# Optimization experiments

Measured on AMD Instinct MI355X. Metric: run time of the kernel, lower is better.

The kernel has to match this reference:

```python
import jax, jax.numpy as jnp
import numpy as np

EPS = 1e-10
W_SILOG, W_L2, W_BINS = 1.0, 1.0, 1.0  # w_masked=1.0 -> invalid branch skipped


def setup_inputs() -> dict:
    key = jax.random.key(0)
    k1, k2, k3, k4 = jax.random.split(key, 4)
    B, H, W = 8, 240, 320
    NB = 256  # n_bins
    prediction = jax.random.uniform(k1, (B, 1, H, W), dtype=jnp.float32)
    target = jax.random.uniform(k2, (B, 1, H, W), dtype=jnp.float32)
    bin_edges = jax.random.uniform(k3, (B, NB + 1), dtype=jnp.float32)
    mask = jax.random.randint(k4, (B, 1, H, W), 0, 2).astype(jnp.bool_)
    return {"prediction": prediction, "target": target, "bin_edges": bin_edges, "mask": mask}


def _onedirectional_dist(a, b):
    # a: [B, Na], b: [B, Nb] -> sum over Na of min_j (a_i - b_j)^2, shape [B]
    d2 = (a[:, :, None] - b[:, None, :]) ** 2  # [B, Na, Nb]
    return jnp.min(d2, axis=2).sum(axis=1)


def reference(prediction, target, bin_edges, mask):
    # Chamfer distance between bin centers and target depth values
    bin_centers = 0.5 * (bin_edges[:, :-1] + bin_edges[:, 1:])  # [B, NB]
    target_depths = target.reshape(target.shape[0], -1)         # [B, H*W]
    chamfer = (_onedirectional_dist(bin_centers, target_depths)
               + _onedirectional_dist(target_depths, bin_centers)).mean()

    # Masked reductions (equivalent to boolean-indexed means, jit-friendly)
    p = prediction.reshape(-1)
    t = target.reshape(-1)
    fm = mask.reshape(-1).astype(p.dtype)
    cnt = fm.sum()

    # L2: sqrt(MSE over masked elements)
    l2 = jnp.sqrt(jnp.sum((p - t) ** 2 * fm) / cnt)

    # SILog
    d = jnp.log(p + EPS) - jnp.log(t + EPS)
    d_mean = jnp.sum(d * fm) / cnt
    d2_mean = jnp.sum(d * d * fm) / cnt
    silog = 10.0 * jnp.sqrt(d2_mean - 0.85 * d_mean ** 2)

    return W_L2 * l2 + W_SILOG * silog + W_BINS * chamfer
```

## Files before the change

### kernel.cpp

```cpp
#include <hip/hip_runtime.h>
#include <math.h>

#define HW     76800
#define NBATCH 8
#define NB     256
#define NEDGE  257
#define ELEMS  12
#define XBLKS  25
#define MAIN_BLOCKS (XBLKS * NBATCH)
#define FINF 3.402823466e+38f


__device__ __forceinline__ double wsum64(double v) {
#pragma unroll
  for (int o = 32; o > 0; o >>= 1) v += __shfl_down(v, o, 64);
  return v;
}

__device__ __forceinline__ unsigned int nzb(unsigned int w) {
  return ((w & 0xFFu) != 0u) + (((w >> 8) & 0xFFu) != 0u) +
         (((w >> 16) & 0xFFu) != 0u) + ((w >> 24) != 0u);
}

__global__ void __launch_bounds__(256) k_prep(
    const float* __restrict__ edges, const unsigned char* __restrict__ mask,
    double* __restrict__ sums, unsigned int* __restrict__ ticket,
    unsigned int* __restrict__ flag, unsigned int* __restrict__ gD,
    float* __restrict__ cs) {
  const int tid = threadIdx.x, b = blockIdx.x;
  if (b < NBATCH) {
    __shared__ float s[NB];
    float v = 0.5f * (edges[b * NEDGE + tid] + edges[b * NEDGE + tid + 1]);
    for (int k = 2; k <= NB; k <<= 1) {
      for (int j = k >> 1; j > 0; j >>= 1) {
        float partner;
        if (j < 64) {
          partner = __shfl_xor(v, j, 64);
        } else {
          __syncthreads();
          s[tid] = v;
          __syncthreads();
          partner = s[tid ^ j];
        }
        const bool up = ((tid & k) == 0);
        const bool low = ((tid & j) == 0);
        v = (low == up) ? fminf(v, partner) : fmaxf(v, partner);
      }
    }
    cs[b * NB + tid] = v;
    gD[b * NB + tid] = 0u;
  } else {
    uint4 raw = ((const uint4*)mask)[tid];
    unsigned int c = nzb(raw.x) + nzb(raw.y) + nzb(raw.z) + nzb(raw.w);
#pragma unroll
    for (int o = 32; o > 0; o >>= 1) c += __shfl_down(c, o, 64);
    __shared__ unsigned int sh[4];
    if ((tid & 63) == 0) sh[tid >> 6] = c;
    __syncthreads();
    if (tid == 0) *flag = ((sh[0] + sh[1] + sh[2] + sh[3]) > 1024u) ? 1u : 0u;
    if (tid < 40) sums[tid] = 0.0;
    if (tid == 40) *ticket = 0u;
  }
}

__global__ void __launch_bounds__(256) k_main(
    const float* __restrict__ p, const float* __restrict__ t,
    const void* __restrict__ mask, const unsigned int* __restrict__ flag,
    const float* __restrict__ cs, double* __restrict__ sums,
    unsigned int* __restrict__ gD, unsigned int* __restrict__ ticket,
    float* __restrict__ out) {
  __shared__ float c_lds[NB];
  __shared__ unsigned int d_lds[NB];
  __shared__ double shred[4][5];
  __shared__ double fin[40];
  __shared__ unsigned int last_flag;

  const int tid = threadIdx.x, lane = tid & 63, wid = tid >> 6;
  const int b = blockIdx.y;
  const int ebase = b * HW + blockIdx.x * (NB * ELEMS) + tid * ELEMS;

  c_lds[tid] = cs[b * NB + tid];
  d_lds[tid] = 0u;
  __syncthreads();
  const float c255 = c_lds[255], c127 = c_lds[127], c63 = c_lds[63],
              c191 = c_lds[191], c31 = c_lds[31], c95 = c_lds[95],
              c159 = c_lds[159], c223 = c_lds[223];

  float pe[ELEMS], te[ELEMS];
  int me[ELEMS];
  {
    const float4* pp = (const float4*)(p + ebase);
    const float4* tt = (const float4*)(t + ebase);
#pragma unroll
    for (int q = 0; q < 3; ++q) {
      float4 a = pp[q], c = tt[q];
      pe[q * 4 + 0] = a.x; pe[q * 4 + 1] = a.y; pe[q * 4 + 2] = a.z; pe[q * 4 + 3] = a.w;
      te[q * 4 + 0] = c.x; te[q * 4 + 1] = c.y; te[q * 4 + 2] = c.z; te[q * 4 + 3] = c.w;
    }
  }
  if (*flag) {
    const unsigned int* mp = (const unsigned int*)((const unsigned char*)mask + ebase);
    unsigned int w[3] = {mp[0], mp[1], mp[2]};
#pragma unroll
    for (int e = 0; e < ELEMS; ++e) me[e] = (w[e >> 2] >> ((e & 3) * 8)) & 0xFFu;
  } else {
    const int4* mp = (const int4*)((const int*)mask + ebase);
#pragma unroll
    for (int q = 0; q < 3; ++q) {
      int4 m4 = mp[q];
      me[q * 4 + 0] = m4.x; me[q * 4 + 1] = m4.y; me[q * 4 + 2] = m4.z; me[q * 4 + 3] = m4.w;
    }
  }

  double cnt = 0, ssq = 0, sd = 0, sd2 = 0, dir2 = 0;
#pragma unroll
  for (int e = 0; e < ELEMS; ++e) {
    const float pi = pe[e], ti = te[e];
    if (me[e]) {
      float diff = pi - ti;
      float d = logf(pi + 1e-10f) - logf(ti + 1e-10f);
      cnt += 1.0;
      ssq += (double)diff * (double)diff;
      sd  += (double)d;
      sd2 += (double)d * (double)d;
    }
    int k = -1;
    if (c127 <= ti) k = 127;
    { float pr = (k == 127) ? c191 : c63; if (pr <= ti) k += 64; }
    { int idx = (k + 32) >> 6;
      float pr = (idx >= 2) ? ((idx == 3) ? c223 : c159)
                            : ((idx == 1) ? c95 : c31);
      if (pr <= ti) k += 32; }
    if (c255 <= ti) k = 255;
#pragma unroll
    for (int s = 16; s > 0; s >>= 1) {
      int nk = k + s;
      if (nk < NB && c_lds[nk] <= ti) k = nk;
    }
    float dl = (k >= 0)     ? ti - c_lds[k]     : FINF;
    float dr = (k + 1 < NB) ? c_lds[k + 1] - ti : FINF;
    if (k >= 0)     atomicMax(&d_lds[k],     ~__float_as_uint(dl));
    if (k + 1 < NB) atomicMax(&d_lds[k + 1], ~__float_as_uint(dr));
    float dmin = fminf(dl, dr);
    dir2 += (double)dmin * (double)dmin;
  }

  __syncthreads();
  {
    unsigned int dv = d_lds[tid];
    if (dv) atomicMax(&gD[b * NB + tid], dv);
  }

  double acc[5] = {cnt, ssq, sd, sd2, dir2};
#pragma unroll
  for (int i = 0; i < 5; ++i) {
    double r = wsum64(acc[i]);
    if (lane == 0) shred[wid][i] = r;
  }
  __syncthreads();
  if (tid < 5) {
    atomicAdd(&sums[b * 5 + tid],
              shred[0][tid] + shred[1][tid] + shred[2][tid] + shred[3][tid]);
  }

  asm volatile("s_waitcnt vmcnt(0) lgkmcnt(0)" ::: "memory");
  __syncthreads();
  if (tid == 0)
    last_flag = (atomicAdd(ticket, 1u) == (unsigned)(MAIN_BLOCKS - 1)) ? 1u : 0u;
  __syncthreads();
  if (last_flag == 0u) return;

  if (tid < 40) fin[tid] = atomicAdd(&sums[tid], 0.0);

  double dir1 = 0.0;
#pragma unroll
  for (int r = 0; r < 2; ++r) {
    const int bb = wid + r * 4;
    float c[4], D[4];
#pragma unroll
    for (int i = 0; i < 4; ++i) {
      const int idx = bb * NB + lane * 4 + i;
      c[i] = cs[idx];
      unsigned int s = atomicOr(&gD[idx], 0u);
      D[i] = s ? __uint_as_float(~s) : FINF;
    }

    float pa[4];
    pa[0] = D[0] - c[0];
    pa[1] = fminf(pa[0], D[1] - c[1]);
    pa[2] = fminf(pa[1], D[2] - c[2]);
    pa[3] = fminf(pa[2], D[3] - c[3]);
    float s1 = pa[3];
#pragma unroll
    for (int off = 1; off < 64; off <<= 1) {
      float u = __shfl_up(s1, off, 64);
      if (lane >= off) s1 = fminf(s1, u);
    }
    float exL = __shfl_up(s1, 1, 64);
    if (lane == 0) exL = FINF;

    float sb[4];
    sb[3] = D[3] + c[3];
    sb[2] = fminf(sb[3], D[2] + c[2]);
    sb[1] = fminf(sb[2], D[1] + c[1]);
    sb[0] = fminf(sb[1], D[0] + c[0]);
    float s2 = sb[0];
#pragma unroll
    for (int off = 1; off < 64; off <<= 1) {
      float u = __shfl_down(s2, off, 64);
      if (lane + off < 64) s2 = fminf(s2, u);
    }
    float exR = __shfl_down(s2, 1, 64);
    if (lane == 63) exR = FINF;

#pragma unroll
    for (int i = 0; i < 4; ++i) {
      float pref = fminf(exL, pa[i]);
      float suf  = fminf(exR, sb[i]);
      float dist = fminf(pref + c[i], suf - c[i]);
      dir1 += (double)dist * (double)dist;
    }
  }

  dir1 = wsum64(dir1);
  if (lane == 0) shred[wid][0] = dir1;
  __syncthreads();
  if (tid == 0) {
    double d1 = shred[0][0] + shred[1][0] + shred[2][0] + shred[3][0];
    double cnt_ = 0, ssq_ = 0, sd_ = 0, sd2_ = 0, d2_ = 0;
#pragma unroll
    for (int bb = 0; bb < NBATCH; ++bb) {
      cnt_ += fin[bb * 5 + 0]; ssq_ += fin[bb * 5 + 1];
      sd_  += fin[bb * 5 + 2]; sd2_ += fin[bb * 5 + 3];
      d2_  += fin[bb * 5 + 4];
    }
    double l2 = sqrt(ssq_ / cnt_);
    double dm = sd_ / cnt_, d2m = sd2_ / cnt_;
    double silog = 10.0 * sqrt(d2m - 0.85 * dm * dm);
    double chamfer = (d1 + d2_) / (double)NBATCH;
    out[0] = (float)(l2 + silog + chamfer);
  }
}

extern "C" void kernel_launch(void* const* d_in, const int* in_sizes, int n_in,
                              void* d_out, int out_size, void* d_ws, size_t ws_size,
                              hipStream_t stream) {
  const float* pred  = (const float*)d_in[0];
  const float* targ  = (const float*)d_in[1];
  const float* edges = (const float*)d_in[2];
  const void*  mask  = d_in[3];

  char* ws = (char*)d_ws;
  double* sums         = (double*)ws;
  unsigned int* ticket = (unsigned int*)(ws + 320);
  unsigned int* flag   = (unsigned int*)(ws + 324);
  unsigned int* gD     = (unsigned int*)(ws + 512);
  float* cs            = (float*)(ws + 8704);

  k_prep<<<NBATCH + 1, NB, 0, stream>>>(edges, (const unsigned char*)mask,
                                        sums, ticket, flag, gD, cs);
  k_main<<<dim3(XBLKS, NBATCH), NB, 0, stream>>>(pred, targ, mask, flag, cs,
                                                 sums, gD, ticket, (float*)d_out);
}
```

Baseline: 24.85 us.

## Replace per-element binary search with uniform-grid LUT and switch accumulators to fp32

The prep kernel now builds, for each batch, a 256-entry lookup table over [0,1) that holds the largest sorted bin center at or below each grid point. The main kernel uses it to jump straight to a nearby bin and walks forward linearly, replacing the 8-step binary search over LDS. Per-thread partial sums and the wave reductions also move from double to float, which cuts FP64 work. This assumes targets lie roughly in [0,1] with evenly spread bin centers (the walk is unbounded if many centers share a cell), and the fp32 accumulation loses some precision.

```diff
diff --git a/kernel.cpp b/kernel.cpp
--- a/kernel.cpp
+++ b/kernel.cpp
@@ -11,7 +11,7 @@
 #define FINF 3.402823466e+38f
 
 
-__device__ __forceinline__ double wsum64(double v) {
+__device__ __forceinline__ float wsum32(float v) {
 #pragma unroll
   for (int o = 32; o > 0; o >>= 1) v += __shfl_down(v, o, 64);
   return v;
@@ -26,7 +26,7 @@
     const float* __restrict__ edges, const unsigned char* __restrict__ mask,
     double* __restrict__ sums, unsigned int* __restrict__ ticket,
     unsigned int* __restrict__ flag, unsigned int* __restrict__ gD,
-    float* __restrict__ cs) {
+    float* __restrict__ cs, float2* __restrict__ gLut) {
   const int tid = threadIdx.x, b = blockIdx.x;
   if (b < NBATCH) {
     __shared__ float s[NB];
@@ -49,6 +49,22 @@
     }
     cs[b * NB + tid] = v;
     gD[b * NB + tid] = 0u;
+    __syncthreads();
+    s[tid] = v;
+    __syncthreads();
+    const float x = (float)tid * 0.00390625f;
+    int k = -1;
+    if (s[255] <= x) {
+      k = 255;
+    } else {
+#pragma unroll
+      for (int st = 128; st > 0; st >>= 1) {
+        int nk = k + st;
+        if (nk < 255 && s[nk] <= x) k = nk;
+      }
+    }
+    float ck = (k >= 0) ? s[k] : -FINF;
+    gLut[b * NB + tid] = make_float2(ck, __int_as_float(k));
   } else {
     uint4 raw = ((const uint4*)mask)[tid];
     unsigned int c = nzb(raw.x) + nzb(raw.y) + nzb(raw.z) + nzb(raw.w);
@@ -66,12 +82,14 @@
 __global__ void __launch_bounds__(256) k_main(
     const float* __restrict__ p, const float* __restrict__ t,
     const void* __restrict__ mask, const unsigned int* __restrict__ flag,
-    const float* __restrict__ cs, double* __restrict__ sums,
-    unsigned int* __restrict__ gD, unsigned int* __restrict__ ticket,
-    float* __restrict__ out) {
-  __shared__ float c_lds[NB];
-  __shared__ unsigned int d_lds[NB];
-  __shared__ double shred[4][5];
+    const float* __restrict__ cs, const float2* __restrict__ gLut,
+    double* __restrict__ sums, unsigned int* __restrict__ gD,
+    unsigned int* __restrict__ ticket, float* __restrict__ out) {
+  __shared__ float c_lds[NB + 1];
+  __shared__ float2 lut_lds[NB];
+  __shared__ unsigned int d_lds[NB + 2];
+  __shared__ float shred[4][5];
+  __shared__ double dpart[4];
   __shared__ double fin[40];
   __shared__ unsigned int last_flag;
 
@@ -80,11 +98,11 @@
   const int ebase = b * HW + blockIdx.x * (NB * ELEMS) + tid * ELEMS;
 
   c_lds[tid] = cs[b * NB + tid];
+  lut_lds[tid] = gLut[b * NB + tid];
   d_lds[tid] = 0u;
-  __syncthreads();
-  const float c255 = c_lds[255], c127 = c_lds[127], c63 = c_lds[63],
-              c191 = c_lds[191], c31 = c_lds[31], c95 = c_lds[95],
-              c159 = c_lds[159], c223 = c_lds[223];
+  if (tid < 2) d_lds[NB + tid] = 0u;
+  if (tid == 0) c_lds[NB] = FINF;
+  __syncthreads();
 
   float pe[ELEMS], te[ELEMS];
   int me[ELEMS];
@@ -112,55 +130,62 @@
     }
   }
 
-  double cnt = 0, ssq = 0, sd = 0, sd2 = 0, dir2 = 0;
+  int cnt = 0;
+  float ssq = 0.f, sd = 0.f, sd2 = 0.f, dir2 = 0.f;
 #pragma unroll
   for (int e = 0; e < ELEMS; ++e) {
-    const float pi = pe[e], ti = te[e];
     if (me[e]) {
-      float diff = pi - ti;
-      float d = logf(pi + 1e-10f) - logf(ti + 1e-10f);
-      cnt += 1.0;
-      ssq += (double)diff * (double)diff;
-      sd  += (double)d;
-      sd2 += (double)d * (double)d;
-    }
-    int k = -1;
-    if (c127 <= ti) k = 127;
-    { float pr = (k == 127) ? c191 : c63; if (pr <= ti) k += 64; }
-    { int idx = (k + 32) >> 6;
-      float pr = (idx >= 2) ? ((idx == 3) ? c223 : c159)
-                            : ((idx == 1) ? c95 : c31);
-      if (pr <= ti) k += 32; }
-    if (c255 <= ti) k = 255;
-#pragma unroll
-    for (int s = 16; s > 0; s >>= 1) {
-      int nk = k + s;
-      if (nk < NB && c_lds[nk] <= ti) k = nk;
-    }
-    float dl = (k >= 0)     ? ti - c_lds[k]     : FINF;
-    float dr = (k + 1 < NB) ? c_lds[k + 1] - ti : FINF;
-    if (k >= 0)     atomicMax(&d_lds[k],     ~__float_as_uint(dl));
-    if (k + 1 < NB) atomicMax(&d_lds[k + 1], ~__float_as_uint(dr));
-    float dmin = fminf(dl, dr);
-    dir2 += (double)dmin * (double)dmin;
+      float diff = pe[e] - te[e];
+      float d = logf(pe[e] + 1e-10f) - logf(te[e] + 1e-10f);
+      cnt += 1;
+      ssq += diff * diff;
+      sd  += d;
+      sd2 += d * d;
+    }
+  }
+
+  int   kk[ELEMS];
+  float ck[ELEMS], c1[ELEMS];
+#pragma unroll
+  for (int e = 0; e < ELEMS; ++e) {
+    int q = (int)(te[e] * 256.0f);
+    q = (q < 0) ? 0 : ((q > 255) ? 255 : q);
+    float2 lu = lut_lds[q];
+    ck[e] = lu.x;
+    kk[e] = __float_as_int(lu.y);
+  }
+#pragma unroll
+  for (int e = 0; e < ELEMS; ++e) c1[e] = c_lds[kk[e] + 1];
+#pragma unroll
+  for (int e = 0; e < ELEMS; ++e) {
+    const float ti = te[e];
+    int k = kk[e];
+    float c0 = ck[e], cn = c1[e];
+    while (cn <= ti) { ++k; c0 = cn; cn = c_lds[k + 1]; }
+    float dl = ti - c0;
+    float dr = cn - ti;
+    atomicMax(&d_lds[k + 1], ~__float_as_uint(dl));
+    atomicMax(&d_lds[k + 2], ~__float_as_uint(dr));
+    float dm = fminf(dl, dr);
+    dir2 += dm * dm;
   }
 
   __syncthreads();
   {
-    unsigned int dv = d_lds[tid];
+    unsigned int dv = d_lds[tid + 1];
     if (dv) atomicMax(&gD[b * NB + tid], dv);
   }
 
-  double acc[5] = {cnt, ssq, sd, sd2, dir2};
+  float acc[5] = {(float)cnt, ssq, sd, sd2, dir2};
 #pragma unroll
   for (int i = 0; i < 5; ++i) {
-    double r = wsum64(acc[i]);
+    float r = wsum32(acc[i]);
     if (lane == 0) shred[wid][i] = r;
   }
   __syncthreads();
   if (tid < 5) {
     atomicAdd(&sums[b * 5 + tid],
-              shred[0][tid] + shred[1][tid] + shred[2][tid] + shred[3][tid]);
+              (double)(shred[0][tid] + shred[1][tid] + shred[2][tid] + shred[3][tid]));
   }
 
   asm volatile("s_waitcnt vmcnt(0) lgkmcnt(0)" ::: "memory");
@@ -222,11 +247,12 @@
     }
   }
 
-  dir1 = wsum64(dir1);
-  if (lane == 0) shred[wid][0] = dir1;
+#pragma unroll
+  for (int o = 32; o > 0; o >>= 1) dir1 += __shfl_down(dir1, o, 64);
+  if (lane == 0) dpart[wid] = dir1;
   __syncthreads();
   if (tid == 0) {
-    double d1 = shred[0][0] + shred[1][0] + shred[2][0] + shred[3][0];
+    double d1 = dpart[0] + dpart[1] + dpart[2] + dpart[3];
     double cnt_ = 0, ssq_ = 0, sd_ = 0, sd2_ = 0, d2_ = 0;
 #pragma unroll
     for (int bb = 0; bb < NBATCH; ++bb) {
@@ -256,9 +282,10 @@
   unsigned int* flag   = (unsigned int*)(ws + 324);
   unsigned int* gD     = (unsigned int*)(ws + 512);
   float* cs            = (float*)(ws + 8704);
+  float2* gLut         = (float2*)(ws + 16896);
 
   k_prep<<<NBATCH + 1, NB, 0, stream>>>(edges, (const unsigned char*)mask,
-                                        sums, ticket, flag, gD, cs);
-  k_main<<<dim3(XBLKS, NBATCH), NB, 0, stream>>>(pred, targ, mask, flag, cs,
+                                        sums, ticket, flag, gD, cs, gLut);
+  k_main<<<dim3(XBLKS, NBATCH), NB, 0, stream>>>(pred, targ, mask, flag, cs, gLut,
                                                  sums, gD, ticket, (float*)d_out);
 }
```

After: 21.72 us. 12.6% less time.
